# Kernel tuning notes

Measured on AMD Instinct MI355X. Metric: run time of the kernel, lower is better.

The kernel has to match this reference:

```python
import jax, jax.numpy as jnp
import numpy as np

D_MODEL = 1024
N_HEADS = 16
HEAD_DIM = D_MODEL // N_HEADS
B, S = 4, 2048


def setup_inputs() -> dict:
    key = jax.random.key(0)
    ks = jax.random.split(key, 12)
    s = 1.0 / np.sqrt(D_MODEL)
    inp = {
        'query': jax.random.normal(ks[0], (B, S, D_MODEL), jnp.float32),
        'key': jax.random.normal(ks[1], (B, S, D_MODEL), jnp.float32),
        'value': jax.random.normal(ks[2], (B, S, D_MODEL), jnp.float32),
        # causal mask, broadcast over batch and heads: [1,1,S,S]
        'mask': jnp.tril(jnp.ones((S, S), jnp.int32))[None, None],
        'Wq': jax.random.normal(ks[3], (D_MODEL, D_MODEL), jnp.float32) * s,
        'bq': jnp.zeros((D_MODEL,), jnp.float32),
        'Wk': jax.random.normal(ks[4], (D_MODEL, D_MODEL), jnp.float32) * s,
        'bk': jnp.zeros((D_MODEL,), jnp.float32),
        'Wv': jax.random.normal(ks[5], (D_MODEL, D_MODEL), jnp.float32) * s,
        'bv': jnp.zeros((D_MODEL,), jnp.float32),
        'Wo': jax.random.normal(ks[6], (D_MODEL, D_MODEL), jnp.float32) * s,
        'bo': jnp.zeros((D_MODEL,), jnp.float32),
    }
    return inp


def reference(query, key, value, mask, Wq, bq, Wk, bk, Wv, bv, Wo, bo):
    b, q_len, _ = query.shape
    scale = jnp.sqrt(jnp.float32(HEAD_DIM))
    # projections
    q = query @ Wq + bq
    k = key @ Wk + bk
    v = value @ Wv + bv
    # [b, h, s, hd]
    q = q.reshape(b, q_len, N_HEADS, HEAD_DIM).transpose(0, 2, 1, 3)
    k = k.reshape(b, -1, N_HEADS, HEAD_DIM).transpose(0, 2, 1, 3)
    v = v.reshape(b, -1, N_HEADS, HEAD_DIM).transpose(0, 2, 1, 3)
    scores = jnp.einsum('bhqd,bhkd->bhqk', q, k) / scale
    scores = jnp.where(mask == 0, jnp.float32(-jnp.inf), scores)
    attn = jax.nn.softmax(scores, axis=-1)  # dropout p=0 / eval mode
    out = jnp.einsum('bhqk,bhkd->bhqd', attn, v)
    out = out.transpose(0, 2, 1, 3).reshape(b, q_len, D_MODEL)
    return out @ Wo + bo
```

## Files before the change

### kernel.cpp

```cpp
#include <hip/hip_runtime.h>
#include <hip/hip_bf16.h>

typedef __attribute__((ext_vector_type(8))) short short8;
typedef __attribute__((ext_vector_type(4))) float floatx4;
typedef __attribute__((ext_vector_type(4))) unsigned short ushort4v;

#define D_MODEL 1024
#define S_LEN   2048
#define N_HEADS 16
#define HEAD_DIM 64
#define BATCH   4

__device__ __forceinline__ unsigned short f2bf(float x) {
    union { float f; unsigned int u; } v; v.f = x;
    unsigned int u = v.u;
    unsigned int r = (u + 0x7FFFu + ((u >> 16) & 1u)) >> 16;
    return (unsigned short)r;
}
__device__ __forceinline__ unsigned short f2bf_trunc(float x) {
    union { float f; unsigned int u; } v; v.f = x;
    return (unsigned short)(v.u >> 16);
}

__device__ __forceinline__ void gload_lds16(const void* g, void* s) {
    __builtin_amdgcn_global_load_lds(
        (const __attribute__((address_space(1))) void*)g,
        (__attribute__((address_space(3))) void*)s, 16, 0, 0);
}

struct Conv3 {
    const float* src[3];
    unsigned short* dst[3];
};

__global__ __launch_bounds__(256) void conv_bf16(Conv3 a) {
    const float* s = a.src[blockIdx.z];
    unsigned short* d = a.dst[blockIdx.z];
    size_t i = ((size_t)blockIdx.x * 256 + threadIdx.x) * 8;
    float4 f0 = *(const float4*)(s + i);
    float4 f1 = *(const float4*)(s + i + 4);
    short8 v;
    v[0] = (short)f2bf(f0.x); v[1] = (short)f2bf(f0.y);
    v[2] = (short)f2bf(f0.z); v[3] = (short)f2bf(f0.w);
    v[4] = (short)f2bf(f1.x); v[5] = (short)f2bf(f1.y);
    v[6] = (short)f2bf(f1.z); v[7] = (short)f2bf(f1.w);
    *(short8*)(d + i) = v;
}

struct Trans4 {
    const float* W[4];
    unsigned short* Wt[4];
};

__global__ __launch_bounds__(256) void transpose_w(Trans4 args) {
    __shared__ unsigned short tile[32][33];
    const float* W = args.W[blockIdx.z];
    unsigned short* Wt = args.Wt[blockIdx.z];
    int n0 = blockIdx.x * 32;
    int k0 = blockIdx.y * 32;
    int t = threadIdx.x;
    int r = t >> 5, c = t & 31;
    for (int i = 0; i < 4; ++i) {
        int k = k0 + r + i * 8;
        tile[r + i * 8][c] = f2bf(W[(size_t)k * D_MODEL + n0 + c]);
    }
    __syncthreads();
    for (int i = 0; i < 4; ++i) {
        int n = n0 + r + i * 8;
        Wt[(size_t)n * D_MODEL + k0 + c] = tile[c][r + i * 8];
    }
}

struct GemmIn {
    const unsigned short* A;
    const unsigned short* Bt;
    const float* bias;
    void* C;
    int mode;
    float scale;
};
struct Gemm3 { GemmIn g[3]; };

#define BAR()   asm volatile("s_barrier" ::: "memory")
#define LGKM0() asm volatile("s_waitcnt lgkmcnt(0)" ::: "memory")
#define VMW4()  asm volatile("s_waitcnt vmcnt(4)" ::: "memory")
#define VMW2()  asm volatile("s_waitcnt vmcnt(2)" ::: "memory")
#define VMW0()  asm volatile("s_waitcnt vmcnt(0)" ::: "memory")

#define READ_A4(BUF)                                                           \
    _Pragma("unroll") for (int ii = 0; ii < 4; ++ii) {                         \
        aF[ii][0] = *(const short8*)&lds[(BUF)*16384 + aOff + ii*512];         \
        aF[ii][1] = *(const short8*)&lds[(BUF)*16384 + aOff + ii*512 + 4096];  \
    }
#define READ_B2(BUF, J0, DST)                                                  \
    _Pragma("unroll") for (int jj = 0; jj < 2; ++jj) {                         \
        DST[jj][0] = *(const short8*)&lds[(BUF)*16384 + bOff + ((J0)+jj)*512]; \
        DST[jj][1] = *(const short8*)&lds[(BUF)*16384 + bOff + ((J0)+jj)*512 + 4096]; \
    }
#define MFMA_H(J0, BREG)                                                       \
    __builtin_amdgcn_s_setprio(1);                                             \
    _Pragma("unroll") for (int ii = 0; ii < 4; ++ii)                           \
    _Pragma("unroll") for (int jj = 0; jj < 2; ++jj) {                         \
        acc[ii][(J0)+jj] = __builtin_amdgcn_mfma_f32_16x16x32_bf16(            \
            aF[ii][0], BREG[jj][0], acc[ii][(J0)+jj], 0, 0, 0);                \
        acc[ii][(J0)+jj] = __builtin_amdgcn_mfma_f32_16x16x32_bf16(            \
            aF[ii][1], BREG[jj][1], acc[ii][(J0)+jj], 0, 0, 0);                \
    }                                                                          \
    __builtin_amdgcn_s_setprio(0)

__global__ __launch_bounds__(256, 2) void gemm_128(Gemm3 args) {
    constexpr int K = D_MODEL, N = D_MODEL;
    constexpr int NT = K / 64;
    constexpr int NI = NT / 2;
    GemmIn g = args.g[blockIdx.z];

    __shared__ __align__(16) unsigned short lds[32768];

    const int m0 = blockIdx.x * 128;
    const int n0 = blockIdx.y * 128;
    const int t = threadIdx.x;
    const int w = t >> 6, lane = t & 63;
    const int quad = lane >> 4, l16 = lane & 15;
    const int wm = w >> 1, wn = w & 1;

    const int srow = w * 32 + (lane >> 2);
    const int scol = ((lane & 3) * 8) ^ ((lane & 32) ? 16 : 0);

    const int fx = (quad * 8) ^ ((l16 & 8) ? 16 : 0);
    const int aOff = (wm * 64 + l16) * 32 + fx;
    const int bOff = 8192 + (wn * 64 + l16) * 32 + fx;

    floatx4 acc[4][4] = {};
    short8 aF[4][2], bE[2][2], bO[2][2];

    auto stageA = [&](int buf, int kt) {
        const unsigned short* s0 = g.A + (size_t)(m0 + srow) * K + kt * 64 + scol;
        unsigned short* d0 = &lds[buf * 16384 + (w * 32) * 32];
        gload_lds16(s0, d0);
        gload_lds16(s0 + 32, d0 + 4096);
        gload_lds16(s0 + (size_t)16 * K, d0 + 512);
        gload_lds16(s0 + (size_t)16 * K + 32, d0 + 512 + 4096);
    };
    auto stageB = [&](int buf, int kt) {
        const unsigned short* s0 = g.Bt + (size_t)(n0 + srow) * K + kt * 64 + scol;
        unsigned short* d0 = &lds[buf * 16384 + 8192 + (w * 32) * 32];
        gload_lds16(s0, d0);
        gload_lds16(s0 + 32, d0 + 4096);
        gload_lds16(s0 + (size_t)16 * K, d0 + 512);
        gload_lds16(s0 + (size_t)16 * K + 32, d0 + 512 + 4096);
    };

    stageA(0, 0); stageB(0, 0);
    VMW0();
    BAR();

    for (int n = 0; n < NI - 1; ++n) {
        const int t0 = 2 * n;
        READ_A4(0); READ_B2(0, 0, bE);
        stageB(1, t0 + 1);
        BAR(); LGKM0();
        MFMA_H(0, bE);
        BAR();
        READ_B2(0, 2, bO);
        stageA(1, t0 + 1);
        BAR(); LGKM0();
        MFMA_H(2, bO);
        VMW0();
        BAR();
        READ_A4(1); READ_B2(1, 0, bE);
        stageB(0, t0 + 2);
        BAR(); LGKM0();
        MFMA_H(0, bE);
        BAR();
        READ_B2(1, 2, bO);
        stageA(0, t0 + 2);
        BAR(); LGKM0();
        MFMA_H(2, bO);
        VMW0();
        BAR();
    }

    {
        READ_A4(0); READ_B2(0, 0, bE);
        stageB(1, NT - 1);
        BAR(); LGKM0();
        MFMA_H(0, bE);
        BAR();
        READ_B2(0, 2, bO);
        stageA(1, NT - 1);
        BAR(); LGKM0();
        MFMA_H(2, bO);
        VMW0();
        BAR();
        READ_A4(1); READ_B2(1, 0, bE);
        BAR(); LGKM0();
        MFMA_H(0, bE);
        BAR();
        READ_B2(1, 2, bO);
        LGKM0();
        MFMA_H(2, bO);
    }

    if (g.mode == 2) {
        unsigned short* Ct = (unsigned short*)g.C;
#pragma unroll
        for (int j = 0; j < 4; ++j) {
            int col = n0 + wn * 64 + j * 16 + l16;
            int h = col >> 6, dd = col & 63;
            float bv = g.bias[col];
#pragma unroll
            for (int i = 0; i < 4; ++i) {
                int row0 = m0 + wm * 64 + i * 16 + quad * 4;
                int bb = row0 >> 11, s = row0 & 2047;
                ushort4v u;
#pragma unroll
                for (int r = 0; r < 4; ++r) u[r] = f2bf((acc[i][j][r] + bv) * g.scale);
                *(ushort4v*)(Ct + ((size_t)(bb * 16 + h) * 64 + dd) * 2048 + s) = u;
            }
        }
    } else {
#pragma unroll
        for (int j = 0; j < 4; ++j) {
            int col = n0 + wn * 64 + j * 16 + l16;
            float bv = g.bias[col];
#pragma unroll
            for (int i = 0; i < 4; ++i) {
#pragma unroll
                for (int r = 0; r < 4; ++r) {
                    int row = m0 + wm * 64 + i * 16 + quad * 4 + r;
                    float v = (acc[i][j][r] + bv) * g.scale;
                    if (g.mode == 1)
                        ((float*)g.C)[(size_t)row * N + col] = v;
                    else
                        ((unsigned short*)g.C)[(size_t)row * N + col] = f2bf(v);
                }
            }
        }
    }
}

__global__ __launch_bounds__(512) void flash_attn(
    const unsigned short* __restrict__ Qp,
    const unsigned short* __restrict__ Kp,
    const unsigned short* __restrict__ Vtg,
    unsigned short* __restrict__ Op) {
    constexpr int S = S_LEN, D = D_MODEL;
    __shared__ __align__(16) unsigned short Ks[3 * 4096];
    __shared__ __align__(16) unsigned short Vs[3 * 4096];
    __shared__ __align__(16) unsigned short Ps[8][1024];

    int id = blockIdx.x + (blockIdx.y << 3);
    int pair = (id >> 3) & 7;
    int bh = (id & 7) | ((id >> 6) << 3);
    int b = bh >> 4;
    int t = threadIdx.x;
    int wave = t >> 6, lane = t & 63;
    int quad = lane >> 4, l16 = lane & 15;

    const size_t head_off = (size_t)b * S * D + (size_t)(bh & 15) * HEAD_DIM;
    const unsigned short* Khead = Kp + head_off;
    const unsigned short* Vhead = Vtg + (size_t)bh * 64 * S;

    int q0l = pair * 128, q0h = (15 - pair) * 128;
    int qgl = q0l + wave * 16 + l16;
    int qgh = q0h + wave * 16 + l16;

    const unsigned short* qpl = Qp + head_off + (size_t)qgl * D + quad * 8;
    short8 ql0 = *(const short8*)qpl, ql1 = *(const short8*)(qpl + 32);
    const unsigned short* qph = Qp + head_off + (size_t)qgh * D + quad * 8;
    short8 qh0 = *(const short8*)qph, qh1 = *(const short8*)(qph + 32);

    floatx4 ol[4] = {}, oh[4] = {};
    floatx4 lsl = {}, lsh = {};

    short8 a1;
#pragma unroll
    for (int e = 0; e < 8; ++e) a1[e] = (l16 == 0) ? (short)0x3F80 : (short)0;

    int sw = wave & 3;
    bool doK = wave < 4;
    int srow = sw * 16 + (lane >> 2);
    int scol = ((lane & 3) * 8) ^ ((lane & 32) ? 16 : 0);

    auto stage = [&](int buf, int k0) {
        if (doK) {
            const unsigned short* s0 = Khead + (size_t)(k0 + srow) * D + scol;
            unsigned short* d0 = Ks + buf * 4096 + sw * 512;
            gload_lds16(s0, d0);
            gload_lds16(s0 + 32, d0 + 2048);
        } else {
            const unsigned short* s0 = Vhead + (size_t)srow * S + k0 + scol;
            unsigned short* d0 = Vs + buf * 4096 + sw * 512;
            gload_lds16(s0, d0);
            gload_lds16(s0 + 32, d0 + 2048);
        }
    };

    int wqminl = q0l + wave * 16, wqmaxl = wqminl + 15;
    int wqminh = q0h + wave * 16, wqmaxh = wqminh + 15;

    const int swz = (quad * 8) ^ ((l16 & 8) ? 16 : 0);
    const int pswz = (l16 & 8) ? 16 : 0;
    unsigned short* pw = &Ps[wave][0];

    auto half_step = [&](const unsigned short* Kb, const unsigned short* Vb,
                         int k0, int qg, int wqmin, floatx4& ls,
                         floatx4* o, short8 qb0, short8 qb1) {
        floatx4 st[4];
        __builtin_amdgcn_s_setprio(1);
        for (int gk = 0; gk < 4; ++gk) {
            short8 ka0 = *(const short8*)&Kb[(gk * 16 + l16) * 32 + swz];
            short8 ka1 = *(const short8*)&Kb[2048 + (gk * 16 + l16) * 32 + swz];
            floatx4 s = {};
            s = __builtin_amdgcn_mfma_f32_16x16x32_bf16(ka0, qb0, s, 0, 0, 0);
            s = __builtin_amdgcn_mfma_f32_16x16x32_bf16(ka1, qb1, s, 0, 0, 0);
            st[gk] = s;
        }
        __builtin_amdgcn_s_setprio(0);

        float sv[16];
        if (k0 + 63 < wqmin) {
            for (int i = 0; i < 16; ++i)
                sv[i] = __builtin_amdgcn_exp2f(st[i >> 2][i & 3]);
        } else {
            for (int gk = 0; gk < 4; ++gk)
                for (int r = 0; r < 4; ++r) {
                    int key = k0 + gk * 16 + quad * 4 + r;
                    sv[gk * 4 + r] = (key <= qg)
                        ? __builtin_amdgcn_exp2f(st[gk][r]) : 0.f;
                }
        }

        for (int gk = 0; gk < 4; ++gk) {
            ushort4v u;
            for (int r = 0; r < 4; ++r) u[r] = f2bf_trunc(sv[gk * 4 + r]);
            *(ushort4v*)&pw[(gk >> 1) * 512 + l16 * 32 +
                            ((((gk & 1) * 16) + quad * 4) ^ pswz)] = u;
        }

        short8 pf0 = *(const short8*)&pw[l16 * 32 + swz];
        short8 pf1 = *(const short8*)&pw[512 + l16 * 32 + swz];
        __builtin_amdgcn_s_setprio(1);
        ls = __builtin_amdgcn_mfma_f32_16x16x32_bf16(a1, pf0, ls, 0, 0, 0);
        ls = __builtin_amdgcn_mfma_f32_16x16x32_bf16(a1, pf1, ls, 0, 0, 0);
        for (int jd = 0; jd < 4; ++jd) {
            short8 va0 = *(const short8*)&Vb[(jd * 16 + l16) * 32 + swz];
            short8 va1 = *(const short8*)&Vb[2048 + (jd * 16 + l16) * 32 + swz];
            o[jd] = __builtin_amdgcn_mfma_f32_16x16x32_bf16(va0, pf0, o[jd], 0, 0, 0);
            o[jd] = __builtin_amdgcn_mfma_f32_16x16x32_bf16(va1, pf1, o[jd], 0, 0, 0);
        }
        __builtin_amdgcn_s_setprio(0);
    };

    int n_kt = 2 * (15 - pair) + 2;
    stage(0, 0);
    stage(1, 64);
    for (int kt = 0; kt < n_kt; ++kt) {
        int k0 = kt * 64;
        if (kt + 2 < n_kt) {
            stage((kt + 2) % 3, k0 + 128);
            VMW4();
        } else if (kt + 1 < n_kt) {
            VMW2();
        } else {
            VMW0();
        }
        BAR();

        const unsigned short* Kb = Ks + (kt % 3) * 4096;
        const unsigned short* Vb = Vs + (kt % 3) * 4096;
        if (k0 <= wqmaxl) half_step(Kb, Vb, k0, qgl, wqminl, lsl, ol, ql0, ql1);
        if (k0 <= wqmaxh) half_step(Kb, Vb, k0, qgh, wqminh, lsh, oh, qh0, qh1);
        BAR();
    }

    {
        float inv = 1.0f / __shfl(lsl[0], l16);
        unsigned short* op = Op + head_off + (size_t)qgl * D;
        for (int jd = 0; jd < 4; ++jd) {
            ushort4v u;
            for (int r = 0; r < 4; ++r) u[r] = f2bf(ol[jd][r] * inv);
            *(ushort4v*)(op + jd * 16 + quad * 4) = u;
        }
    }
    {
        float inv = 1.0f / __shfl(lsh[0], l16);
        unsigned short* op = Op + head_off + (size_t)qgh * D;
        for (int jd = 0; jd < 4; ++jd) {
            ushort4v u;
            for (int r = 0; r < 4; ++r) u[r] = f2bf(oh[jd][r] * inv);
            *(ushort4v*)(op + jd * 16 + quad * 4) = u;
        }
    }
}

extern "C" void kernel_launch(void* const* d_in, const int* in_sizes, int n_in,
                              void* d_out, int out_size, void* d_ws,
                              size_t ws_size, hipStream_t stream) {
    const float* query = (const float*)d_in[0];
    const float* key   = (const float*)d_in[1];
    const float* value = (const float*)d_in[2];
    const float* Wq = (const float*)d_in[4];
    const float* bq = (const float*)d_in[5];
    const float* Wk = (const float*)d_in[6];
    const float* bk = (const float*)d_in[7];
    const float* Wv = (const float*)d_in[8];
    const float* bv = (const float*)d_in[9];
    const float* Wo = (const float*)d_in[10];
    const float* bo = (const float*)d_in[11];
    float* out = (float*)d_out;

    char* ws = (char*)d_ws;
    const size_t WT_SZ = (size_t)D_MODEL * D_MODEL * 2;
    const size_t X_SZ = (size_t)BATCH * S_LEN * D_MODEL * 2;
    unsigned short* wtq = (unsigned short*)(ws);
    unsigned short* wtk = (unsigned short*)(ws + WT_SZ);
    unsigned short* wtv = (unsigned short*)(ws + 2 * WT_SZ);
    unsigned short* wto = (unsigned short*)(ws + 3 * WT_SZ);
    unsigned short* Qbf = (unsigned short*)(ws + 4 * WT_SZ);
    unsigned short* Kbf = (unsigned short*)(ws + 4 * WT_SZ + X_SZ);
    unsigned short* Vbf = (unsigned short*)(ws + 4 * WT_SZ + 2 * X_SZ);
    unsigned short* Qp  = (unsigned short*)(ws + 4 * WT_SZ + 3 * X_SZ);
    unsigned short* Kp  = (unsigned short*)(ws + 4 * WT_SZ + 4 * X_SZ);
    unsigned short* Vtg = (unsigned short*)(ws + 4 * WT_SZ + 5 * X_SZ);
    unsigned short* Ao  = Qbf;

    Trans4 ta;
    ta.W[0] = Wq; ta.W[1] = Wk; ta.W[2] = Wv; ta.W[3] = Wo;
    ta.Wt[0] = wtq; ta.Wt[1] = wtk; ta.Wt[2] = wtv; ta.Wt[3] = wto;
    transpose_w<<<dim3(32, 32, 4), 256, 0, stream>>>(ta);

    Conv3 ca;
    ca.src[0] = query; ca.src[1] = key; ca.src[2] = value;
    ca.dst[0] = Qbf;   ca.dst[1] = Kbf; ca.dst[2] = Vbf;
    conv_bf16<<<dim3(4096, 1, 3), 256, 0, stream>>>(ca);

    const float q_scale = 0.125f * 1.44269504088896340736f;
    Gemm3 gq;
    gq.g[0].A = Qbf; gq.g[0].Bt = wtq; gq.g[0].bias = bq; gq.g[0].C = Qp;  gq.g[0].mode = 0; gq.g[0].scale = q_scale;
    gq.g[1].A = Kbf; gq.g[1].Bt = wtk; gq.g[1].bias = bk; gq.g[1].C = Kp;  gq.g[1].mode = 0; gq.g[1].scale = 1.0f;
    gq.g[2].A = Vbf; gq.g[2].Bt = wtv; gq.g[2].bias = bv; gq.g[2].C = Vtg; gq.g[2].mode = 2; gq.g[2].scale = 1.0f;
    gemm_128<<<dim3(64, 8, 3), 256, 0, stream>>>(gq);

    flash_attn<<<dim3(8, BATCH * N_HEADS), 512, 0, stream>>>(
        Qp, Kp, Vtg, Ao);

    Gemm3 go;
    go.g[0].A = Ao; go.g[0].Bt = wto; go.g[0].bias = bo; go.g[0].C = out; go.g[0].mode = 1; go.g[0].scale = 1.0f;
    gemm_128<<<dim3(64, 8, 1), 256, 0, stream>>>(go);
}
```

Measured before the change: 306.8 us.

## Merge prep kernels into one launch and simplify GEMM K-loop pipeline

Merges the weight-transpose and input bf16-conversion kernels into a single launch, where blockIdx.z selects the task and surplus transpose blocks exit early. Replaces the hand-interleaved GEMM main loop, which split B fragment reads and MFMAs into halves between barriers, with a plain double-buffered loop. That loop prefetches the next tile, reads all fragments, runs all MFMAs, then waits and takes one barrier. This saves a launch and barrier overhead but gives up the finer interleaving of LDS reads, global prefetch and MFMA work.

```diff
diff --git a/kernel.cpp b/kernel.cpp
--- a/kernel.cpp
+++ b/kernel.cpp
@@ -28,46 +28,45 @@
         (__attribute__((address_space(3))) void*)s, 16, 0, 0);
 }
 
-struct Conv3 {
-    const float* src[3];
-    unsigned short* dst[3];
-};
-
-__global__ __launch_bounds__(256) void conv_bf16(Conv3 a) {
-    const float* s = a.src[blockIdx.z];
-    unsigned short* d = a.dst[blockIdx.z];
-    size_t i = ((size_t)blockIdx.x * 256 + threadIdx.x) * 8;
-    float4 f0 = *(const float4*)(s + i);
-    float4 f1 = *(const float4*)(s + i + 4);
-    short8 v;
-    v[0] = (short)f2bf(f0.x); v[1] = (short)f2bf(f0.y);
-    v[2] = (short)f2bf(f0.z); v[3] = (short)f2bf(f0.w);
-    v[4] = (short)f2bf(f1.x); v[5] = (short)f2bf(f1.y);
-    v[6] = (short)f2bf(f1.z); v[7] = (short)f2bf(f1.w);
-    *(short8*)(d + i) = v;
-}
-
-struct Trans4 {
+struct Prep {
+    const float* csrc[3];
+    unsigned short* cdst[3];
     const float* W[4];
     unsigned short* Wt[4];
 };
 
-__global__ __launch_bounds__(256) void transpose_w(Trans4 args) {
+__global__ __launch_bounds__(256) void prep(Prep a) {
     __shared__ unsigned short tile[32][33];
-    const float* W = args.W[blockIdx.z];
-    unsigned short* Wt = args.Wt[blockIdx.z];
-    int n0 = blockIdx.x * 32;
-    int k0 = blockIdx.y * 32;
-    int t = threadIdx.x;
-    int r = t >> 5, c = t & 31;
-    for (int i = 0; i < 4; ++i) {
-        int k = k0 + r + i * 8;
-        tile[r + i * 8][c] = f2bf(W[(size_t)k * D_MODEL + n0 + c]);
-    }
-    __syncthreads();
-    for (int i = 0; i < 4; ++i) {
-        int n = n0 + r + i * 8;
-        Wt[(size_t)n * D_MODEL + k0 + c] = tile[c][r + i * 8];
+    int z = blockIdx.z;
+    if (z < 3) {
+        const float* s = a.csrc[z];
+        unsigned short* d = a.cdst[z];
+        size_t i = ((size_t)blockIdx.x * 256 + threadIdx.x) * 8;
+        float4 f0 = *(const float4*)(s + i);
+        float4 f1 = *(const float4*)(s + i + 4);
+        short8 v;
+        v[0] = (short)f2bf(f0.x); v[1] = (short)f2bf(f0.y);
+        v[2] = (short)f2bf(f0.z); v[3] = (short)f2bf(f0.w);
+        v[4] = (short)f2bf(f1.x); v[5] = (short)f2bf(f1.y);
+        v[6] = (short)f2bf(f1.z); v[7] = (short)f2bf(f1.w);
+        *(short8*)(d + i) = v;
+    } else {
+        if (blockIdx.x >= 1024) return;
+        const float* W = a.W[z - 3];
+        unsigned short* Wt = a.Wt[z - 3];
+        int n0 = (blockIdx.x & 31) * 32;
+        int k0 = (blockIdx.x >> 5) * 32;
+        int t = threadIdx.x;
+        int r = t >> 5, c = t & 31;
+        for (int i = 0; i < 4; ++i) {
+            int k = k0 + r + i * 8;
+            tile[r + i * 8][c] = f2bf(W[(size_t)k * D_MODEL + n0 + c]);
+        }
+        __syncthreads();
+        for (int i = 0; i < 4; ++i) {
+            int n = n0 + r + i * 8;
+            Wt[(size_t)n * D_MODEL + k0 + c] = tile[c][r + i * 8];
+        }
     }
 }
 
@@ -92,26 +91,25 @@
         aF[ii][0] = *(const short8*)&lds[(BUF)*16384 + aOff + ii*512];         \
         aF[ii][1] = *(const short8*)&lds[(BUF)*16384 + aOff + ii*512 + 4096];  \
     }
-#define READ_B2(BUF, J0, DST)                                                  \
-    _Pragma("unroll") for (int jj = 0; jj < 2; ++jj) {                         \
-        DST[jj][0] = *(const short8*)&lds[(BUF)*16384 + bOff + ((J0)+jj)*512]; \
-        DST[jj][1] = *(const short8*)&lds[(BUF)*16384 + bOff + ((J0)+jj)*512 + 4096]; \
-    }
-#define MFMA_H(J0, BREG)                                                       \
+#define READ_B4(BUF)                                                           \
+    _Pragma("unroll") for (int jj = 0; jj < 4; ++jj) {                         \
+        bF[jj][0] = *(const short8*)&lds[(BUF)*16384 + bOff + jj*512];         \
+        bF[jj][1] = *(const short8*)&lds[(BUF)*16384 + bOff + jj*512 + 4096];  \
+    }
+#define MFMA_ALL()                                                             \
     __builtin_amdgcn_s_setprio(1);                                             \
     _Pragma("unroll") for (int ii = 0; ii < 4; ++ii)                           \
-    _Pragma("unroll") for (int jj = 0; jj < 2; ++jj) {                         \
-        acc[ii][(J0)+jj] = __builtin_amdgcn_mfma_f32_16x16x32_bf16(            \
-            aF[ii][0], BREG[jj][0], acc[ii][(J0)+jj], 0, 0, 0);                \
-        acc[ii][(J0)+jj] = __builtin_amdgcn_mfma_f32_16x16x32_bf16(            \
-            aF[ii][1], BREG[jj][1], acc[ii][(J0)+jj], 0, 0, 0);                \
+    _Pragma("unroll") for (int jj = 0; jj < 4; ++jj) {                         \
+        acc[ii][jj] = __builtin_amdgcn_mfma_f32_16x16x32_bf16(                 \
+            aF[ii][0], bF[jj][0], acc[ii][jj], 0, 0, 0);                       \
+        acc[ii][jj] = __builtin_amdgcn_mfma_f32_16x16x32_bf16(                 \
+            aF[ii][1], bF[jj][1], acc[ii][jj], 0, 0, 0);                       \
     }                                                                          \
     __builtin_amdgcn_s_setprio(0)
 
 __global__ __launch_bounds__(256, 2) void gemm_128(Gemm3 args) {
     constexpr int K = D_MODEL, N = D_MODEL;
     constexpr int NT = K / 64;
-    constexpr int NI = NT / 2;
     GemmIn g = args.g[blockIdx.z];
 
     __shared__ __align__(16) unsigned short lds[32768];
@@ -131,7 +129,7 @@
     const int bOff = 8192 + (wn * 64 + l16) * 32 + fx;
 
     floatx4 acc[4][4] = {};
-    short8 aF[4][2], bE[2][2], bO[2][2];
+    short8 aF[4][2], bF[4][2];
 
     auto stageA = [&](int buf, int kt) {
         const unsigned short* s0 = g.A + (size_t)(m0 + srow) * K + kt * 64 + scol;
@@ -154,51 +152,14 @@
     VMW0();
     BAR();
 
-    for (int n = 0; n < NI - 1; ++n) {
-        const int t0 = 2 * n;
-        READ_A4(0); READ_B2(0, 0, bE);
-        stageB(1, t0 + 1);
-        BAR(); LGKM0();
-        MFMA_H(0, bE);
-        BAR();
-        READ_B2(0, 2, bO);
-        stageA(1, t0 + 1);
-        BAR(); LGKM0();
-        MFMA_H(2, bO);
-        VMW0();
-        BAR();
-        READ_A4(1); READ_B2(1, 0, bE);
-        stageB(0, t0 + 2);
-        BAR(); LGKM0();
-        MFMA_H(0, bE);
-        BAR();
-        READ_B2(1, 2, bO);
-        stageA(0, t0 + 2);
-        BAR(); LGKM0();
-        MFMA_H(2, bO);
-        VMW0();
-        BAR();
-    }
-
-    {
-        READ_A4(0); READ_B2(0, 0, bE);
-        stageB(1, NT - 1);
-        BAR(); LGKM0();
-        MFMA_H(0, bE);
-        BAR();
-        READ_B2(0, 2, bO);
-        stageA(1, NT - 1);
-        BAR(); LGKM0();
-        MFMA_H(2, bO);
-        VMW0();
-        BAR();
-        READ_A4(1); READ_B2(1, 0, bE);
-        BAR(); LGKM0();
-        MFMA_H(0, bE);
-        BAR();
-        READ_B2(1, 2, bO);
+#pragma unroll 2
+    for (int kt = 0; kt < NT; ++kt) {
+        const int buf = kt & 1;
+        if (kt + 1 < NT) { stageA(buf ^ 1, kt + 1); stageB(buf ^ 1, kt + 1); }
+        READ_A4(buf); READ_B4(buf);
         LGKM0();
-        MFMA_H(2, bO);
+        MFMA_ALL();
+        if (kt + 1 < NT) { VMW0(); BAR(); }
     }
 
     if (g.mode == 2) {
@@ -425,15 +386,12 @@
     unsigned short* Vtg = (unsigned short*)(ws + 4 * WT_SZ + 5 * X_SZ);
     unsigned short* Ao  = Qbf;
 
-    Trans4 ta;
-    ta.W[0] = Wq; ta.W[1] = Wk; ta.W[2] = Wv; ta.W[3] = Wo;
-    ta.Wt[0] = wtq; ta.Wt[1] = wtk; ta.Wt[2] = wtv; ta.Wt[3] = wto;
-    transpose_w<<<dim3(32, 32, 4), 256, 0, stream>>>(ta);
-
-    Conv3 ca;
-    ca.src[0] = query; ca.src[1] = key; ca.src[2] = value;
-    ca.dst[0] = Qbf;   ca.dst[1] = Kbf; ca.dst[2] = Vbf;
-    conv_bf16<<<dim3(4096, 1, 3), 256, 0, stream>>>(ca);
+    Prep pa;
+    pa.csrc[0] = query; pa.csrc[1] = key; pa.csrc[2] = value;
+    pa.cdst[0] = Qbf;   pa.cdst[1] = Kbf; pa.cdst[2] = Vbf;
+    pa.W[0] = Wq; pa.W[1] = Wk; pa.W[2] = Wv; pa.W[3] = Wo;
+    pa.Wt[0] = wtq; pa.Wt[1] = wtk; pa.Wt[2] = wtv; pa.Wt[3] = wto;
+    prep<<<dim3(4096, 1, 7), 256, 0, stream>>>(pa);
 
     const float q_scale = 0.125f * 1.44269504088896340736f;
     Gemm3 gq;
```

Measured after the change: 315.8 us. 1.03x slower.
